# Performance work log

Measured on AMD Instinct MI355X. Metric: run time of the kernel, lower is better.

Reference implementation:

```python
import jax, jax.numpy as jnp
import numpy as np

B, S, H = 16, 2048, 1024

def setup_inputs() -> dict:
    key = jax.random.key(0)
    k1, k2, k3, k4, k5 = jax.random.split(key, 5)
    hidden = jax.random.normal(k1, (B, 1, H), dtype=jnp.float32)
    encoder_outputs = jax.random.normal(k2, (B, S, H), dtype=jnp.float32)
    # nn.Linear(2H -> H): weight [H, 2H], bias [H]
    lim = 1.0 / np.sqrt(2 * H)
    attn_w = jax.random.uniform(k3, (H, 2 * H), minval=-lim, maxval=lim, dtype=jnp.float32)
    attn_b = jax.random.uniform(k4, (H,), minval=-lim, maxval=lim, dtype=jnp.float32)
    v = jax.random.normal(k5, (1, H), dtype=jnp.float32)
    return {"hidden": hidden, "encoder_outputs": encoder_outputs,
            "attn_w": attn_w, "attn_b": attn_b, "v": v}

def reference(hidden, encoder_outputs, attn_w, attn_b, v):
    # hidden: [B,1,H] broadcast across seq; encoder_outputs: [B,S,H]
    Bc, Sc, Hc = encoder_outputs.shape
    h = jnp.broadcast_to(hidden, (Bc, Sc, Hc))
    x = jnp.concatenate([h, encoder_outputs], axis=-1)        # [B,S,2H]
    energy = jnp.einsum('bsk,hk->bsh', x, attn_w) + attn_b    # [B,S,H]
    scores = jnp.einsum('bsh,h->bs', energy, v[0])            # [B,S]
    return jax.nn.softmax(scores, axis=-1)[:, None, :]        # [B,1,S]
```

## Files before the change

### kernel.cpp

```cpp
#include <hip/hip_runtime.h>
#include <math.h>

#define BATCH 16
#define SEQ   2048
#define HID   1024

__global__ __launch_bounds__(256) void we_partial_kernel(
    const float* __restrict__ attn_w,
    const float* __restrict__ v,
    float* __restrict__ partial)
{
    const int tid   = threadIdx.x;
    const int chunk = blockIdx.x;
    const int h0    = chunk * 8;

    float4 acc = make_float4(0.f, 0.f, 0.f, 0.f);
#pragma unroll
    for (int r = 0; r < 8; ++r) {
        const int h = h0 + r;
        const float vh = v[h];
        const float4 a =
            ((const float4*)(attn_w + (size_t)h * (2 * HID) + HID))[tid];
        acc.x += vh * a.x;
        acc.y += vh * a.y;
        acc.z += vh * a.z;
        acc.w += vh * a.w;
    }
    ((float4*)(partial + (size_t)chunk * HID))[tid] = acc;
}

__global__ __launch_bounds__(256) void we_reduce_kernel(
    const float* __restrict__ partial,
    float* __restrict__ w2)
{
    const int j = blockIdx.x * 256 + threadIdx.x;
    float acc = 0.f;
#pragma unroll 8
    for (int y = 0; y < 128; ++y)
        acc += partial[(size_t)y * HID + j];
    w2[j] = acc;
}

__global__ __launch_bounds__(256) void scores_kernel(
    const float* __restrict__ enc,
    const float* __restrict__ w2,
    float* __restrict__ scores)
{
    const int wave = (int)((blockIdx.x * 256 + threadIdx.x) >> 6);
    const int lane = threadIdx.x & 63;

    float4 w[4];
#pragma unroll
    for (int c = 0; c < 4; ++c)
        w[c] = ((const float4*)w2)[c * 64 + lane];

    float a0 = 0.f, a1 = 0.f, a2 = 0.f, a3 = 0.f;
    const float4* rp0 = (const float4*)(enc + (size_t)(wave * 4 + 0) * HID);
    const float4* rp1 = (const float4*)(enc + (size_t)(wave * 4 + 1) * HID);
    const float4* rp2 = (const float4*)(enc + (size_t)(wave * 4 + 2) * HID);
    const float4* rp3 = (const float4*)(enc + (size_t)(wave * 4 + 3) * HID);

#pragma unroll
    for (int c = 0; c < 4; ++c) {
        const float4 e0 = rp0[c * 64 + lane];
        const float4 e1 = rp1[c * 64 + lane];
        const float4 e2 = rp2[c * 64 + lane];
        const float4 e3 = rp3[c * 64 + lane];
        a0 += e0.x * w[c].x + e0.y * w[c].y + e0.z * w[c].z + e0.w * w[c].w;
        a1 += e1.x * w[c].x + e1.y * w[c].y + e1.z * w[c].z + e1.w * w[c].w;
        a2 += e2.x * w[c].x + e2.y * w[c].y + e2.z * w[c].z + e2.w * w[c].w;
        a3 += e3.x * w[c].x + e3.y * w[c].y + e3.z * w[c].z + e3.w * w[c].w;
    }

#pragma unroll
    for (int off = 32; off > 0; off >>= 1) {
        a0 += __shfl_xor(a0, off, 64);
        a1 += __shfl_xor(a1, off, 64);
        a2 += __shfl_xor(a2, off, 64);
        a3 += __shfl_xor(a3, off, 64);
    }

    if (lane < 4) {
        const float val = (lane == 0) ? a0 : (lane == 1) ? a1
                        : (lane == 2) ? a2 : a3;
        scores[wave * 4 + lane] = val;
    }
}

__global__ __launch_bounds__(256) void softmax_kernel(
    const float* __restrict__ scores,
    float* __restrict__ out)
{
    const int b   = blockIdx.x;
    const int tid = threadIdx.x;
    const float* s = scores + (size_t)b * SEQ;

    __shared__ float red[256];

    float local[8];
    float m = -INFINITY;
#pragma unroll
    for (int i = 0; i < 8; ++i) {
        local[i] = s[tid + i * 256];
        m = fmaxf(m, local[i]);
    }
    red[tid] = m;
    __syncthreads();
    for (int st = 128; st > 0; st >>= 1) {
        if (tid < st) red[tid] = fmaxf(red[tid], red[tid + st]);
        __syncthreads();
    }
    m = red[0];
    __syncthreads();

    float e[8];
    float sum = 0.f;
#pragma unroll
    for (int i = 0; i < 8; ++i) {
        e[i] = __expf(local[i] - m);
        sum += e[i];
    }
    red[tid] = sum;
    __syncthreads();
    for (int st = 128; st > 0; st >>= 1) {
        if (tid < st) red[tid] += red[tid + st];
        __syncthreads();
    }
    const float inv = 1.f / red[0];
#pragma unroll
    for (int i = 0; i < 8; ++i)
        out[(size_t)b * SEQ + tid + i * 256] = e[i] * inv;
}

extern "C" void kernel_launch(void* const* d_in, const int* in_sizes, int n_in,
                              void* d_out, int out_size, void* d_ws, size_t ws_size,
                              hipStream_t stream)
{
    const float* enc    = (const float*)d_in[1];
    const float* attn_w = (const float*)d_in[2];
    const float* v      = (const float*)d_in[4];

    float* ws      = (float*)d_ws;
    float* w2      = ws;
    float* partial = ws + HID;
    float* scores  = ws + HID + 128 * HID;

    we_partial_kernel<<<128, 256, 0, stream>>>(attn_w, v, partial);
    we_reduce_kernel <<<4,   256, 0, stream>>>(partial, w2);
    scores_kernel    <<<2048, 256, 0, stream>>>(enc, w2, scores);
    softmax_kernel   <<<BATCH, 256, 0, stream>>>(scores, (float*)d_out);
}
```

Baseline: 214.9 us.

## Fuse softmax into scores kernel via last-block atomic counter; merge weight reduction

Collapses the two-kernel w2 = v·W_enc computation into one kernel that reduces across rows in shared memory, and fuses the softmax into the scores kernel. The last of the 128 blocks covering each batch row, detected with an atomic counter, performs the softmax. This removes two kernel launches and the partial-sum round trip, at the cost of a threadfence and atomic per block and a tail where only 16 blocks run the softmax. The counter reset in the first kernel relies on stream ordering between the two launches.

Result: slower. 576.5 us (+168.3%).

```diff
diff --git a/kernel.cpp b/kernel.cpp
--- a/kernel.cpp
+++ b/kernel.cpp
@@ -5,49 +5,58 @@
 #define SEQ   2048
 #define HID   1024
 
-__global__ __launch_bounds__(256) void we_partial_kernel(
+__global__ __launch_bounds__(256) void we_kernel(
     const float* __restrict__ attn_w,
     const float* __restrict__ v,
-    float* __restrict__ partial)
+    float* __restrict__ w2,
+    int* __restrict__ cnt)
 {
-    const int tid   = threadIdx.x;
-    const int chunk = blockIdx.x;
-    const int h0    = chunk * 8;
+    const int tid = threadIdx.x;
+    const int bid = blockIdx.x;
 
-    float4 acc = make_float4(0.f, 0.f, 0.f, 0.f);
-#pragma unroll
-    for (int r = 0; r < 8; ++r) {
-        const int h = h0 + r;
-        const float vh = v[h];
-        const float4 a =
-            ((const float4*)(attn_w + (size_t)h * (2 * HID) + HID))[tid];
-        acc.x += vh * a.x;
-        acc.y += vh * a.y;
-        acc.z += vh * a.z;
-        acc.w += vh * a.w;
+    if (bid == 0 && tid < BATCH)
+        cnt[tid] = 0;
+
+    __shared__ float vs[HID];
+    __shared__ float red[256];
+
+    for (int i = tid; i < HID; i += 256)
+        vs[i] = v[i];
+    __syncthreads();
+
+    const int c = tid & 15;
+    const int g = tid >> 4;
+    const int j = bid * 16 + c;
+
+    float acc = 0.f;
+#pragma unroll 16
+    for (int k = 0; k < 64; ++k) {
+        const int h = g * 64 + k;
+        acc += vs[h] * attn_w[(size_t)h * (2 * HID) + HID + j];
     }
-    ((float4*)(partial + (size_t)chunk * HID))[tid] = acc;
+    red[tid] = acc;
+    __syncthreads();
+
+    if (tid < 128) red[tid] += red[tid + 128];
+    __syncthreads();
+    if (tid < 64)  red[tid] += red[tid + 64];
+    __syncthreads();
+    if (tid < 32)  red[tid] += red[tid + 32];
+    __syncthreads();
+    if (tid < 16)
+        w2[bid * 16 + tid] = red[tid] + red[tid + 16];
 }
 
-__global__ __launch_bounds__(256) void we_reduce_kernel(
-    const float* __restrict__ partial,
-    float* __restrict__ w2)
-{
-    const int j = blockIdx.x * 256 + threadIdx.x;
-    float acc = 0.f;
-#pragma unroll 8
-    for (int y = 0; y < 128; ++y)
-        acc += partial[(size_t)y * HID + j];
-    w2[j] = acc;
-}
-
-__global__ __launch_bounds__(256) void scores_kernel(
+__global__ __launch_bounds__(256) void scores_softmax_kernel(
     const float* __restrict__ enc,
     const float* __restrict__ w2,
-    float* __restrict__ scores)
+    float* __restrict__ scores,
+    int* __restrict__ cnt,
+    float* __restrict__ out)
 {
-    const int wave = (int)((blockIdx.x * 256 + threadIdx.x) >> 6);
-    const int lane = threadIdx.x & 63;
+    const int tid  = threadIdx.x;
+    const int wave = (int)((blockIdx.x * 256 + tid) >> 6);
+    const int lane = tid & 63;
 
     float4 w[4];
 #pragma unroll
@@ -85,17 +94,22 @@
                         : (lane == 2) ? a2 : a3;
         scores[wave * 4 + lane] = val;
     }
-}
 
-__global__ __launch_bounds__(256) void softmax_kernel(
-    const float* __restrict__ scores,
-    float* __restrict__ out)
-{
-    const int b   = blockIdx.x;
-    const int tid = threadIdx.x;
+    __threadfence();
+    __syncthreads();
+
+    __shared__ int lastFlag;
+    __shared__ float red[256];
+    const int b = blockIdx.x >> 7;
+    if (tid == 0) {
+        const int t = atomicAdd(&cnt[b], 1);
+        lastFlag = (t == 127);
+        if (t == 127) __threadfence();
+    }
+    __syncthreads();
+    if (!lastFlag) return;
+
     const float* s = scores + (size_t)b * SEQ;
-
-    __shared__ float red[256];
 
     float local[8];
     float m = -INFINITY;
@@ -140,13 +154,12 @@
     const float* attn_w = (const float*)d_in[2];
     const float* v      = (const float*)d_in[4];
 
-    float* ws      = (float*)d_ws;
-    float* w2      = ws;
-    float* partial = ws + HID;
-    float* scores  = ws + HID + 128 * HID;
+    float* ws     = (float*)d_ws;
+    float* w2     = ws;
+    int*   cnt    = (int*)(ws + HID);
+    float* scores = ws + HID + 128 * HID;
 
-    we_partial_kernel<<<128, 256, 0, stream>>>(attn_w, v, partial);
-    we_reduce_kernel <<<4,   256, 0, stream>>>(partial, w2);
-    scores_kernel    <<<2048, 256, 0, stream>>>(enc, w2, scores);
-    softmax_kernel   <<<BATCH, 256, 0, stream>>>(scores, (float*)d_out);
+    we_kernel            <<<64,   256, 0, stream>>>(attn_w, v, w2, cnt);
+    scores_softmax_kernel<<<2048, 256, 0, stream>>>(enc, w2, scores, cnt,
+                                                    (float*)d_out);
 }
```
